# Kernel tuning notes

Measured on AMD Instinct MI355X. Metric: run time of the kernel, lower is better.

## Reference

```python
import jax, jax.numpy as jnp
import numpy as np

B, N = 256, 512          # trees, nodes per tree (topological order, root last)
IN, HID, OUT = 57, 512, 57  # len(ascii_letters + " .,;'") = 57


def setup_inputs() -> dict:
    rng = np.random.default_rng(0)
    # children indices strictly less than node index; -1 means absent child
    u = rng.random((B, N, 2))
    idx = np.arange(N)[None, :, None]
    ch = np.floor(u * (idx + 1)).astype(np.int32) - 1  # in [-1, i-1]
    left_idx = jnp.asarray(ch[..., 0])
    right_idx = jnp.asarray(ch[..., 1])
    values = jnp.asarray(rng.integers(0, IN, (B, N)), dtype=jnp.int32)
    key = jax.random.key(0)
    k1, k2, k3, k4 = jax.random.split(key, 4)
    s1 = 1.0 / np.sqrt(IN + HID)
    s2 = 1.0 / np.sqrt(HID)
    W_ih = jax.random.uniform(k1, (IN + HID, HID), minval=-s1, maxval=s1, dtype=jnp.float32)
    b_ih = jax.random.uniform(k2, (HID,), minval=-s1, maxval=s1, dtype=jnp.float32)
    W_o = jax.random.uniform(k3, (HID, OUT), minval=-s2, maxval=s2, dtype=jnp.float32)
    b_o = jax.random.uniform(k4, (OUT,), minval=-s2, maxval=s2, dtype=jnp.float32)
    return dict(left_idx=left_idx, right_idx=right_idx, values=values,
                W_ih=W_ih, b_ih=b_ih, W_o=W_o, b_o=b_o)


def _encode(left_idx, right_idx, values, W_ih, b_ih):
    # one-hot chars, precompute the input half of the concat+linear for all nodes
    X = jax.nn.one_hot(values, IN, dtype=W_ih.dtype)        # [B,N,IN]
    Wx, Wh = W_ih[:IN], W_ih[IN:]                            # split concat linear
    Xp = jnp.einsum('bni,ih->bnh', X, Wx) + b_ih             # [B,N,HID]
    SENT = N  # sentinel row holding zeros (hidden for None child)
    li = jnp.where(left_idx < 0, SENT, left_idx)             # [B,N]
    ri = jnp.where(right_idx < 0, SENT, right_idx)
    H0 = jnp.zeros((B, N + 1, HID), Xp.dtype)
    brange = jnp.arange(B)

    def step(H, inp):
        i, xp, l, r = inp                                    # xp:[B,HID], l/r:[B]
        hl = H[brange, l]                                    # gather child hiddens
        hr = H[brange, r]
        h = jnp.tanh(xp + (hl + hr) @ Wh)                    # recurrence
        H = H.at[:, i].set(h)
        return H, None

    xs = (jnp.arange(N), jnp.swapaxes(Xp, 0, 1), li.T, ri.T)
    H, _ = jax.lax.scan(step, H0, xs)
    return H[:, N - 1]                                       # root hidden [B,HID]


def reference(left_idx, right_idx, values, W_ih, b_ih, W_o, b_o):
    h_root = _encode(left_idx, right_idx, values, W_ih, b_ih)
    logits = h_root @ W_o + b_o                              # i2o
    return jax.nn.log_softmax(logits, axis=1)                # [B,OUT]
```

## Files before the change

### kernel.cpp

```cpp
#include <hip/hip_runtime.h>
#include <stdint.h>
#include <math.h>

#define BATCH 256
#define NNODE 512
#define INP   57
#define HIDD  512
#define OUTD  57
#define SENTOFF (NNODE * HIDD)

typedef int i32x4 __attribute__((ext_vector_type(4)));

__global__ void pack_wq(const float* __restrict__ W_ih, const float* __restrict__ b_ih,
                        signed char* __restrict__ Wq){
  int idx = blockIdx.x * 256 + threadIdx.x;
  int j    =  idx        & 15;
  int lane = (idx >> 4)  & 63;
  int nt   = (idx >> 10) & 31;
  int kt   =  idx >> 15;
  int n    = nt * 16 + (lane & 15);
  int ksub = (lane >> 4) * 16 + j;
  const float scale = 127.0f * sqrtf((float)(INP + HIDD));
  float wv; float sc = scale;
  if (kt < 8) {
    const int ktrue = kt * 64 + 16 * (ksub & 3) + (ksub >> 2);
    wv = W_ih[(size_t)(INP + ktrue) * HIDD + n];
  } else {
    sc = scale * 0.5f;
    if (ksub < INP)       wv = W_ih[(size_t)ksub * HIDD + n];
    else if (ksub == INP) wv = b_ih[n];
    else                  wv = 0.0f;
  }
  float q = rintf(wv * sc);
  q = fminf(127.0f, fmaxf(-127.0f, q));
  Wq[idx] = (signed char)q;
}

__device__ __forceinline__ unsigned int avg_s8x4(unsigned int a, unsigned int b){
  unsigned int au = a ^ 0x80808080u, bu = b ^ 0x80808080u;
  unsigned int o = au | bu, x = au ^ bu;
  return ((o - ((x >> 1) & 0x7F7F7F7Fu)) ^ 0x80808080u);
}

struct Pref { uint4 l[2]; uint4 r[2]; };

__device__ __forceinline__ void load_pref_safe(
    Pref& p, int m0, int Mcur, int w, int m16, int quad,
    const int* ord_s, const int* li_s, const int* ri_s, const int* hot_s,
    const signed char* Hb)
{
  const int koff = w * 64 + quad * 16;
  #pragma unroll
  for (int mt = 0; mt < 2; ++mt) {
    const int row  = mt * 16 + m16;
    const bool live = row < Mcur;
    const int pos  = m0 + row;
    const int node = live ? ord_s[pos] : -1;
    const int hb   = live ? hot_s[pos] : 0;
    const int loff = (node >= 0) ? li_s[node] : SENTOFF;
    const int roff = (node >= 0) ? ri_s[node] : SENTOFF;
    if (!(hb & 1)) p.l[mt] = *(const uint4*)(Hb + (size_t)(loff + koff));
    if (!(hb & 2)) p.r[mt] = *(const uint4*)(Hb + (size_t)(roff + koff));
  }
}

__device__ __forceinline__ void write_pref(
    const Pref& p, int m0, int Mcur, int w, int lane, int m16, int quad,
    signed char* __restrict__ Ab, const int* ord_s, const int* val_s)
{
  #pragma unroll
  for (int mt = 0; mt < 2; ++mt) {
    uint4 o;
    o.x = avg_s8x4(p.l[mt].x, p.r[mt].x);
    o.y = avg_s8x4(p.l[mt].y, p.r[mt].y);
    o.z = avg_s8x4(p.l[mt].z, p.r[mt].z);
    o.w = avg_s8x4(p.l[mt].w, p.r[mt].w);
    *(uint4*)(Ab + (w * 2 + mt) * 1024 + lane * 16) = o;
  }
  if (w < 2) {
    const int erow  = w * 16 + m16;
    const int enode = (erow < Mcur) ? ord_s[m0 + erow] : -1;
    const int v     = (enode >= 0) ? val_s[enode] : -1;
    signed char bytes[16];
    #pragma unroll
    for (int j = 0; j < 16; ++j) {
      const int ks = quad * 16 + j;
      bytes[j] = (enode >= 0 && (ks == v || ks == INP)) ? (signed char)127 : (signed char)0;
    }
    *(i32x4*)(Ab + (16 + w) * 1024 + lane * 16) = *(const i32x4*)bytes;
  }
}

__device__ __forceinline__ void patch_and_write(
    Pref& p, int m0, int Mcur, int w, int lane, int m16, int quad,
    signed char* __restrict__ Ab,
    const int* ord_s, const int* li_s, const int* ri_s, const int* val_s,
    const int* hot_s, const signed char* Hb)
{
  const int koff = w * 64 + quad * 16;
  #pragma unroll
  for (int mt = 0; mt < 2; ++mt) {
    const int row  = mt * 16 + m16;
    const bool live = row < Mcur;
    const int pos  = m0 + row;
    const int hb   = live ? hot_s[pos] : 0;
    if (hb) {
      const int node = ord_s[pos];
      if (hb & 1) p.l[mt] = *(const uint4*)(Hb + (size_t)(li_s[node] + koff));
      if (hb & 2) p.r[mt] = *(const uint4*)(Hb + (size_t)(ri_s[node] + koff));
    }
  }
  write_pref(p, m0, Mcur, w, lane, m16, quad, Ab, ord_s, val_s);
}

#define VSCALE_VAL (2.0f / (16129.0f * 23.853720883753127f))

__device__ __forceinline__ int tanh_q_lut(int accv, const signed char* lut){
  int idx = (accv + 655872) >> 10;
  idx = min(max(idx, 0), 1279);
  return lut[idx];
}

template<int NMT>
__device__ __forceinline__ void compute_chunk(
    int m0, int Mcur, int w, int lane, int m16, int quad,
    const signed char* __restrict__ Ab,
    const int* ordoff_s, const i32x4 (&Bv)[9][4], signed char* Hb,
    const signed char* __restrict__ lut)
{
  i32x4 acc[NMT][4];
  #pragma unroll
  for (int mt = 0; mt < NMT; ++mt)
    #pragma unroll
    for (int nt = 0; nt < 4; ++nt)
      acc[mt][nt] = (i32x4){0, 0, 0, 0};

  #pragma unroll
  for (int kt = 0; kt < 8; ++kt) {
    #pragma unroll
    for (int mt = 0; mt < NMT; ++mt) {
      i32x4 a = *(const i32x4*)(Ab + (kt * 2 + mt) * 1024 + lane * 16);
      #pragma unroll
      for (int nt = 0; nt < 4; ++nt)
        acc[mt][nt] = __builtin_amdgcn_mfma_i32_16x16x64_i8(a, Bv[kt][nt], acc[mt][nt], 0, 0, 0);
    }
  }
  #pragma unroll
  for (int mt = 0; mt < NMT; ++mt) {
    i32x4 ax = *(const i32x4*)(Ab + (16 + mt) * 1024 + lane * 16);
    #pragma unroll
    for (int nt = 0; nt < 4; ++nt)
      acc[mt][nt] = __builtin_amdgcn_mfma_i32_16x16x64_i8(ax, Bv[8][nt], acc[mt][nt], 0, 0, 0);
  }

  #pragma unroll
  for (int mt = 0; mt < NMT; ++mt) {
    #pragma unroll
    for (int rg = 0; rg < 4; ++rg) {
      const int rowc = mt * 16 + quad * 4 + rg;
      if (rowc < Mcur) {
        const int q0 = tanh_q_lut(acc[mt][0][rg], lut) & 255;
        const int q1 = tanh_q_lut(acc[mt][1][rg], lut) & 255;
        const int q2 = tanh_q_lut(acc[mt][2][rg], lut) & 255;
        const int q3 = tanh_q_lut(acc[mt][3][rg], lut);
        const int packed = q0 | (q1 << 8) | (q2 << 16) | (q3 << 24);
        *(int*)(Hb + (size_t)ordoff_s[m0 + rowc] + (w * 64 + m16 * 4)) = packed;
      }
    }
  }
}

__global__ __launch_bounds__(512, 2) void tree_rnn(
    const int* __restrict__ left, const int* __restrict__ right,
    const int* __restrict__ values,
    const float* __restrict__ W_ih, const float* __restrict__ b_ih,
    const float* __restrict__ W_o,  const float* __restrict__ b_o,
    const signed char* __restrict__ Wq,
    signed char* __restrict__ Hbuf, float* __restrict__ out)
{
  __shared__ __align__(16) signed char Abuf[2][18 * 1024];
  __shared__ signed char tanhlut_s[1280];
  __shared__ int li_s[NNODE], ri_s[NNODE], val_s[NNODE];
  __shared__ int lvl_s[NNODE], ord_s[NNODE], ordoff_s[NNODE], hot_s[NNODE];
  __shared__ int cnt_s[NNODE], cnt2_s[NNODE];
  __shared__ int offs_s[NNODE + 1];
  __shared__ int cdesc_s[NNODE];
  __shared__ int chg_s, lmax_s, nc_s;
  __shared__ float hroot_s[HIDD];
  __shared__ float red_s[OUTD][8];
  __shared__ float logit_s[64];

  const int b    = blockIdx.x;
  const int tid  = threadIdx.x;
  const int lane = tid & 63;
  const int w    = tid >> 6;
  signed char* Hb = Hbuf + (size_t)b * (NNODE + 1) * HIDD;

  li_s[tid]  = left  [b * NNODE + tid];
  ri_s[tid]  = right [b * NNODE + tid];
  val_s[tid] = values[b * NNODE + tid];
  lvl_s[tid] = 0; cnt_s[tid] = 0; cnt2_s[tid] = 0;
  if (tid < 128) ((unsigned int*)(Hb + (size_t)NNODE * HIDD))[tid] = 0;
  if (tid == 0) lmax_s = 0;
  for (int i = tid; i < 1280; i += 512) {
    const float xc = (float)((i << 10) - 655360) * VSCALE_VAL;
    tanhlut_s[i] = (signed char)__float2int_rn(127.0f * tanhf(xc));
  }
  __syncthreads();

  for (;;) {
    if (tid == 0) chg_s = 0;
    __syncthreads();
    {
      int l = li_s[tid], r = ri_s[tid];
      int dl = (l >= 0) ? lvl_s[l] : -1;
      int dr = (r >= 0) ? lvl_s[r] : -1;
      int nl = 1 + (dl > dr ? dl : dr);
      if (nl > lvl_s[tid]) { lvl_s[tid] = nl; chg_s = 1; }
    }
    __syncthreads();
    if (!chg_s) break;
  }

  const int myl = lvl_s[tid];
  {
    int ml = myl;
    #pragma unroll
    for (int m = 1; m < 64; m <<= 1) ml = max(ml, __shfl_xor(ml, m, 64));
    if (lane == 0) atomicMax(&lmax_s, ml);
    atomicAdd(&cnt_s[myl], 1);
  }
  __syncthreads();
  const int Lmax = lmax_s;
  if (tid == 0) {
    int acc = 0;
    for (int L = 0; L <= Lmax; ++L) { offs_s[L] = acc; acc += cnt_s[L]; }
    offs_s[Lmax + 1] = acc;
    int nc = 0;
    for (int L = 0; L <= Lmax; ++L)
      for (int m0 = offs_s[L]; m0 < offs_s[L + 1]; m0 += 32) {
        int sz = min(32, offs_s[L + 1] - m0);
        cdesc_s[nc++] = m0 | (sz << 16) | ((m0 == offs_s[L]) ? (1 << 30) : 0);
      }
    nc_s = nc;
  }
  __syncthreads();
  {
    int pos = offs_s[myl] + atomicAdd(&cnt2_s[myl], 1);
    ord_s[pos] = tid;
    ordoff_s[pos] = tid * HIDD;
  }
  __syncthreads();
  {
    const int node = ord_s[tid];
    const int L = lvl_s[node];
    const int l = li_s[node], r = ri_s[node];
    const bool first = (tid - offs_s[L]) < 32;
    int h = 0;
    if (first && l >= 0 && lvl_s[l] == L - 1) h |= 1;
    if (first && r >= 0 && lvl_s[r] == L - 1) h |= 2;
    hot_s[tid] = h;
  }
  __syncthreads();
  {
    int l = li_s[tid], r = ri_s[tid];
    li_s[tid] = (l < 0 ? NNODE : l) * HIDD;
    ri_s[tid] = (r < 0 ? NNODE : r) * HIDD;
  }
  __syncthreads();

  const int m16  = lane & 15;
  const int quad = lane >> 4;

  i32x4 Bv[9][4];
  #pragma unroll
  for (int kt = 0; kt < 9; ++kt)
    #pragma unroll
    for (int nt = 0; nt < 4; ++nt)
      Bv[kt][nt] = *(const i32x4*)(Wq + ((size_t)(kt * 32 + 4 * w + nt) * 64 + lane) * 16);

  const int NC = nc_s;
  Pref p;
  {
    const int d = cdesc_s[0];
    load_pref_safe(p, d & 0xFFFF, (d >> 16) & 0x3FFF, w, m16, quad,
                   ord_s, li_s, ri_s, hot_s, Hb);
  }
  for (int gc = 0; gc < NC; ++gc) {
    const int d  = cdesc_s[gc];
    const int m0 = d & 0xFFFF, Mc = (d >> 16) & 0x3FFF;
    const bool first = (d >> 30) & 1;
    __syncthreads();
    if (first) {
      patch_and_write(p, m0, Mc, w, lane, m16, quad, Abuf[gc & 1],
                      ord_s, li_s, ri_s, val_s, hot_s, Hb);
      __syncthreads();
    }
    const bool more = gc + 1 < NC;
    Pref pn; int m01 = 0, Mc1 = 0; bool f1 = false;
    if (more) {
      const int d1 = cdesc_s[gc + 1];
      m01 = d1 & 0xFFFF; Mc1 = (d1 >> 16) & 0x3FFF; f1 = (d1 >> 30) & 1;
      load_pref_safe(pn, m01, Mc1, w, m16, quad, ord_s, li_s, ri_s, hot_s, Hb);
    }
    const signed char* Ab = Abuf[gc & 1];
    if (Mc > 16)
      compute_chunk<2>(m0, Mc, w, lane, m16, quad, Ab, ordoff_s, Bv, Hb, tanhlut_s);
    else
      compute_chunk<1>(m0, Mc, w, lane, m16, quad, Ab, ordoff_s, Bv, Hb, tanhlut_s);
    if (more && !f1)
      write_pref(pn, m01, Mc1, w, lane, m16, quad, Abuf[(gc + 1) & 1], ord_s, val_s);
    p = pn;
  }
  __syncthreads();

  {
    const int t6 = tid & 63;
    const int tt = (tid & ~63) | (((t6 & 3) << 4) | (t6 >> 2));
    hroot_s[tt] = (float)Hb[(size_t)(NNODE - 1) * HIDD + tid] * (1.0f / 127.0f);
  }
  __syncthreads();
  {
    const int j = tid >> 3, part = tid & 7;
    if (j < OUTD) {
      float p2 = 0.f;
      const int k0 = part * 64;
      for (int k = k0; k < k0 + 64; ++k)
        p2 += hroot_s[k] * W_o[(size_t)k * OUTD + j];
      red_s[j][part] = p2;
    }
  }
  __syncthreads();
  if (tid < OUTD) {
    float s = b_o[tid];
    #pragma unroll
    for (int pp = 0; pp < 8; ++pp) s += red_s[tid][pp];
    logit_s[tid] = s;
  }
  __syncthreads();
  if (w == 0) {
    float x = (lane < OUTD) ? logit_s[lane] : -1e30f;
    float mx = x;
    #pragma unroll
    for (int m = 1; m < 64; m <<= 1) mx = fmaxf(mx, __shfl_xor(mx, m, 64));
    float ex = (lane < OUTD) ? __expf(x - mx) : 0.f;
    float sm = ex;
    #pragma unroll
    for (int m = 1; m < 64; m <<= 1) sm += __shfl_xor(sm, m, 64);
    float ls = logf(sm);
    if (lane < OUTD) out[b * OUTD + lane] = x - mx - ls;
  }
}

extern "C" void kernel_launch(void* const* d_in, const int* in_sizes, int n_in,
                              void* d_out, int out_size, void* d_ws, size_t ws_size,
                              hipStream_t stream) {
  const int*   left   = (const int*)  d_in[0];
  const int*   right  = (const int*)  d_in[1];
  const int*   values = (const int*)  d_in[2];
  const float* W_ih   = (const float*)d_in[3];
  const float* b_ih   = (const float*)d_in[4];
  const float* W_o    = (const float*)d_in[5];
  const float* b_o    = (const float*)d_in[6];
  float* out = (float*)d_out;

  signed char* Wq   = (signed char*)d_ws;
  signed char* Hbuf = (signed char*)((char*)d_ws + 512 * 1024);

  pack_wq<<<1152, 256, 0, stream>>>(W_ih, b_ih, Wq);
  tree_rnn<<<BATCH, 512, 0, stream>>>(left, right, values, W_ih, b_ih, W_o, b_o,
                                      Wq, Hbuf, out);
}
```

Baseline: 199.0 us.

## Process two trees per workgroup and interleave their level chunks

Each workgroup now handles two trees, loading the quantized weight fragments into registers once and interleaving the chunk computations of both trees inside one loop with shared barriers. The intent is to amortize the per-block weight register load and the barrier latency across two independent recurrences, so the memory and sync stalls of one tree can be hidden by work on the other. The cost is half as many blocks (128 on a GPU with many more CUs), doubled LDS use, and serialized work per block, which may leave much of the device idle.

```diff
diff --git a/kernel.cpp b/kernel.cpp
--- a/kernel.cpp
+++ b/kernel.cpp
@@ -178,14 +178,14 @@
     const signed char* __restrict__ Wq,
     signed char* __restrict__ Hbuf, float* __restrict__ out)
 {
-  __shared__ __align__(16) signed char Abuf[2][18 * 1024];
+  __shared__ __align__(16) signed char Abuf[2][2][18 * 1024];
   __shared__ signed char tanhlut_s[1280];
-  __shared__ int li_s[NNODE], ri_s[NNODE], val_s[NNODE];
-  __shared__ int lvl_s[NNODE], ord_s[NNODE], ordoff_s[NNODE], hot_s[NNODE];
-  __shared__ int cnt_s[NNODE], cnt2_s[NNODE];
-  __shared__ int offs_s[NNODE + 1];
-  __shared__ int cdesc_s[NNODE];
-  __shared__ int chg_s, lmax_s, nc_s;
+  __shared__ int li_s[2][NNODE], ri_s[2][NNODE], val_s[2][NNODE];
+  __shared__ int lvl_s[2][NNODE], ord_s[2][NNODE], ordoff_s[2][NNODE], hot_s[2][NNODE];
+  __shared__ int cnt_s[2][NNODE], cnt2_s[2][NNODE];
+  __shared__ int offs_s[2][NNODE + 1];
+  __shared__ int cdesc_s[2][NNODE];
+  __shared__ int chg_s, lmax_s[2], nc_s[2];
   __shared__ float hroot_s[HIDD];
   __shared__ float red_s[OUTD][8];
   __shared__ float logit_s[64];
@@ -194,14 +194,20 @@
   const int tid  = threadIdx.x;
   const int lane = tid & 63;
   const int w    = tid >> 6;
-  signed char* Hb = Hbuf + (size_t)b * (NNODE + 1) * HIDD;
-
-  li_s[tid]  = left  [b * NNODE + tid];
-  ri_s[tid]  = right [b * NNODE + tid];
-  val_s[tid] = values[b * NNODE + tid];
-  lvl_s[tid] = 0; cnt_s[tid] = 0; cnt2_s[tid] = 0;
-  if (tid < 128) ((unsigned int*)(Hb + (size_t)NNODE * HIDD))[tid] = 0;
-  if (tid == 0) lmax_s = 0;
+  signed char* HbT[2] = {
+    Hbuf + (size_t)(2 * b)     * (NNODE + 1) * HIDD,
+    Hbuf + (size_t)(2 * b + 1) * (NNODE + 1) * HIDD };
+
+  #pragma unroll
+  for (int t = 0; t < 2; ++t) {
+    const int r = (2 * b + t) * NNODE + tid;
+    li_s[t][tid]  = left[r];
+    ri_s[t][tid]  = right[r];
+    val_s[t][tid] = values[r];
+    lvl_s[t][tid] = 0; cnt_s[t][tid] = 0; cnt2_s[t][tid] = 0;
+    if (tid < 128) ((unsigned int*)(HbT[t] + (size_t)NNODE * HIDD))[tid] = 0;
+  }
+  if (tid < 2) lmax_s[tid] = 0;
   for (int i = tid; i < 1280; i += 512) {
     const float xc = (float)((i << 10) - 655360) * VSCALE_VAL;
     tanhlut_s[i] = (signed char)__float2int_rn(127.0f * tanhf(xc));
@@ -211,61 +217,69 @@
   for (;;) {
     if (tid == 0) chg_s = 0;
     __syncthreads();
-    {
-      int l = li_s[tid], r = ri_s[tid];
-      int dl = (l >= 0) ? lvl_s[l] : -1;
-      int dr = (r >= 0) ? lvl_s[r] : -1;
+    int any = 0;
+    #pragma unroll
+    for (int t = 0; t < 2; ++t) {
+      int l = li_s[t][tid], r = ri_s[t][tid];
+      int dl = (l >= 0) ? lvl_s[t][l] : -1;
+      int dr = (r >= 0) ? lvl_s[t][r] : -1;
       int nl = 1 + (dl > dr ? dl : dr);
-      if (nl > lvl_s[tid]) { lvl_s[tid] = nl; chg_s = 1; }
-    }
+      if (nl > lvl_s[t][tid]) { lvl_s[t][tid] = nl; any = 1; }
+    }
+    if (any) chg_s = 1;
     __syncthreads();
     if (!chg_s) break;
   }
 
-  const int myl = lvl_s[tid];
-  {
-    int ml = myl;
+  #pragma unroll
+  for (int t = 0; t < 2; ++t) {
+    int ml = lvl_s[t][tid];
     #pragma unroll
     for (int m = 1; m < 64; m <<= 1) ml = max(ml, __shfl_xor(ml, m, 64));
-    if (lane == 0) atomicMax(&lmax_s, ml);
-    atomicAdd(&cnt_s[myl], 1);
-  }
-  __syncthreads();
-  const int Lmax = lmax_s;
-  if (tid == 0) {
+    if (lane == 0) atomicMax(&lmax_s[t], ml);
+    atomicAdd(&cnt_s[t][lvl_s[t][tid]], 1);
+  }
+  __syncthreads();
+  if (tid < 2) {
+    const int t = tid;
     int acc = 0;
-    for (int L = 0; L <= Lmax; ++L) { offs_s[L] = acc; acc += cnt_s[L]; }
-    offs_s[Lmax + 1] = acc;
+    const int Lm = lmax_s[t];
+    for (int L = 0; L <= Lm; ++L) { offs_s[t][L] = acc; acc += cnt_s[t][L]; }
+    offs_s[t][Lm + 1] = acc;
     int nc = 0;
-    for (int L = 0; L <= Lmax; ++L)
-      for (int m0 = offs_s[L]; m0 < offs_s[L + 1]; m0 += 32) {
-        int sz = min(32, offs_s[L + 1] - m0);
-        cdesc_s[nc++] = m0 | (sz << 16) | ((m0 == offs_s[L]) ? (1 << 30) : 0);
+    for (int L = 0; L <= Lm; ++L)
+      for (int m0 = offs_s[t][L]; m0 < offs_s[t][L + 1]; m0 += 32) {
+        int sz = min(32, offs_s[t][L + 1] - m0);
+        cdesc_s[t][nc++] = m0 | (sz << 16) | ((m0 == offs_s[t][L]) ? (1 << 30) : 0);
       }
-    nc_s = nc;
-  }
-  __syncthreads();
-  {
-    int pos = offs_s[myl] + atomicAdd(&cnt2_s[myl], 1);
-    ord_s[pos] = tid;
-    ordoff_s[pos] = tid * HIDD;
-  }
-  __syncthreads();
-  {
-    const int node = ord_s[tid];
-    const int L = lvl_s[node];
-    const int l = li_s[node], r = ri_s[node];
-    const bool first = (tid - offs_s[L]) < 32;
+    nc_s[t] = nc;
+  }
+  __syncthreads();
+  #pragma unroll
+  for (int t = 0; t < 2; ++t) {
+    const int myl = lvl_s[t][tid];
+    int pos = offs_s[t][myl] + atomicAdd(&cnt2_s[t][myl], 1);
+    ord_s[t][pos] = tid;
+    ordoff_s[t][pos] = tid * HIDD;
+  }
+  __syncthreads();
+  #pragma unroll
+  for (int t = 0; t < 2; ++t) {
+    const int node = ord_s[t][tid];
+    const int L = lvl_s[t][node];
+    const int l = li_s[t][node], r = ri_s[t][node];
+    const bool first = (tid - offs_s[t][L]) < 32;
     int h = 0;
-    if (first && l >= 0 && lvl_s[l] == L - 1) h |= 1;
-    if (first && r >= 0 && lvl_s[r] == L - 1) h |= 2;
-    hot_s[tid] = h;
-  }
-  __syncthreads();
-  {
-    int l = li_s[tid], r = ri_s[tid];
-    li_s[tid] = (l < 0 ? NNODE : l) * HIDD;
-    ri_s[tid] = (r < 0 ? NNODE : r) * HIDD;
+    if (first && l >= 0 && lvl_s[t][l] == L - 1) h |= 1;
+    if (first && r >= 0 && lvl_s[t][r] == L - 1) h |= 2;
+    hot_s[t][tid] = h;
+  }
+  __syncthreads();
+  #pragma unroll
+  for (int t = 0; t < 2; ++t) {
+    int l = li_s[t][tid], r = ri_s[t][tid];
+    li_s[t][tid] = (l < 0 ? NNODE : l) * HIDD;
+    ri_s[t][tid] = (r < 0 ? NNODE : r) * HIDD;
   }
   __syncthreads();
 
@@ -279,76 +293,110 @@
     for (int nt = 0; nt < 4; ++nt)
       Bv[kt][nt] = *(const i32x4*)(Wq + ((size_t)(kt * 32 + 4 * w + nt) * 64 + lane) * 16);
 
-  const int NC = nc_s;
-  Pref p;
+  const int NCa = nc_s[0], NCb = nc_s[1];
+  const int NC = max(NCa, NCb);
+  Pref pA, pB;
   {
-    const int d = cdesc_s[0];
-    load_pref_safe(p, d & 0xFFFF, (d >> 16) & 0x3FFF, w, m16, quad,
-                   ord_s, li_s, ri_s, hot_s, Hb);
+    const int d = cdesc_s[0][0];
+    load_pref_safe(pA, d & 0xFFFF, (d >> 16) & 0x3FFF, w, m16, quad,
+                   ord_s[0], li_s[0], ri_s[0], hot_s[0], HbT[0]);
+    const int e = cdesc_s[1][0];
+    load_pref_safe(pB, e & 0xFFFF, (e >> 16) & 0x3FFF, w, m16, quad,
+                   ord_s[1], li_s[1], ri_s[1], hot_s[1], HbT[1]);
   }
   for (int gc = 0; gc < NC; ++gc) {
-    const int d  = cdesc_s[gc];
-    const int m0 = d & 0xFFFF, Mc = (d >> 16) & 0x3FFF;
-    const bool first = (d >> 30) & 1;
-    __syncthreads();
-    if (first) {
-      patch_and_write(p, m0, Mc, w, lane, m16, quad, Abuf[gc & 1],
-                      ord_s, li_s, ri_s, val_s, hot_s, Hb);
-      __syncthreads();
-    }
-    const bool more = gc + 1 < NC;
-    Pref pn; int m01 = 0, Mc1 = 0; bool f1 = false;
-    if (more) {
-      const int d1 = cdesc_s[gc + 1];
-      m01 = d1 & 0xFFFF; Mc1 = (d1 >> 16) & 0x3FFF; f1 = (d1 >> 30) & 1;
-      load_pref_safe(pn, m01, Mc1, w, m16, quad, ord_s, li_s, ri_s, hot_s, Hb);
-    }
-    const signed char* Ab = Abuf[gc & 1];
-    if (Mc > 16)
-      compute_chunk<2>(m0, Mc, w, lane, m16, quad, Ab, ordoff_s, Bv, Hb, tanhlut_s);
-    else
-      compute_chunk<1>(m0, Mc, w, lane, m16, quad, Ab, ordoff_s, Bv, Hb, tanhlut_s);
-    if (more && !f1)
-      write_pref(pn, m01, Mc1, w, lane, m16, quad, Abuf[(gc + 1) & 1], ord_s, val_s);
-    p = pn;
-  }
-  __syncthreads();
-
-  {
-    const int t6 = tid & 63;
-    const int tt = (tid & ~63) | (((t6 & 3) << 4) | (t6 >> 2));
-    hroot_s[tt] = (float)Hb[(size_t)(NNODE - 1) * HIDD + tid] * (1.0f / 127.0f);
-  }
-  __syncthreads();
-  {
-    const int j = tid >> 3, part = tid & 7;
-    if (j < OUTD) {
-      float p2 = 0.f;
-      const int k0 = part * 64;
-      for (int k = k0; k < k0 + 64; ++k)
-        p2 += hroot_s[k] * W_o[(size_t)k * OUTD + j];
-      red_s[j][part] = p2;
-    }
-  }
-  __syncthreads();
-  if (tid < OUTD) {
-    float s = b_o[tid];
-    #pragma unroll
-    for (int pp = 0; pp < 8; ++pp) s += red_s[tid][pp];
-    logit_s[tid] = s;
-  }
-  __syncthreads();
-  if (w == 0) {
-    float x = (lane < OUTD) ? logit_s[lane] : -1e30f;
-    float mx = x;
-    #pragma unroll
-    for (int m = 1; m < 64; m <<= 1) mx = fmaxf(mx, __shfl_xor(mx, m, 64));
-    float ex = (lane < OUTD) ? __expf(x - mx) : 0.f;
-    float sm = ex;
-    #pragma unroll
-    for (int m = 1; m < 64; m <<= 1) sm += __shfl_xor(sm, m, 64);
-    float ls = logf(sm);
-    if (lane < OUTD) out[b * OUTD + lane] = x - mx - ls;
+    const int dA = (gc < NCa) ? cdesc_s[0][gc] : 0;
+    const int dB = (gc < NCb) ? cdesc_s[1][gc] : 0;
+    const bool fA = (gc < NCa) && ((dA >> 30) & 1);
+    const bool fB = (gc < NCb) && ((dB >> 30) & 1);
+    __syncthreads();
+    if (fA) patch_and_write(pA, dA & 0xFFFF, (dA >> 16) & 0x3FFF, w, lane, m16, quad,
+                            &Abuf[0][gc & 1][0], ord_s[0], li_s[0], ri_s[0],
+                            val_s[0], hot_s[0], HbT[0]);
+    if (fB) patch_and_write(pB, dB & 0xFFFF, (dB >> 16) & 0x3FFF, w, lane, m16, quad,
+                            &Abuf[1][gc & 1][0], ord_s[1], li_s[1], ri_s[1],
+                            val_s[1], hot_s[1], HbT[1]);
+    if (fA | fB) __syncthreads();
+
+    if (gc < NCa) {
+      const int m0 = dA & 0xFFFF, Mc = (dA >> 16) & 0x3FFF;
+      const bool more = gc + 1 < NCa;
+      int m01 = 0, Mc1 = 0; bool f1 = false;
+      if (more) {
+        const int d1 = cdesc_s[0][gc + 1];
+        m01 = d1 & 0xFFFF; Mc1 = (d1 >> 16) & 0x3FFF; f1 = (d1 >> 30) & 1;
+        load_pref_safe(pA, m01, Mc1, w, m16, quad,
+                       ord_s[0], li_s[0], ri_s[0], hot_s[0], HbT[0]);
+      }
+      const signed char* Ab = &Abuf[0][gc & 1][0];
+      if (Mc > 16)
+        compute_chunk<2>(m0, Mc, w, lane, m16, quad, Ab, ordoff_s[0], Bv, HbT[0], tanhlut_s);
+      else
+        compute_chunk<1>(m0, Mc, w, lane, m16, quad, Ab, ordoff_s[0], Bv, HbT[0], tanhlut_s);
+      if (more && !f1)
+        write_pref(pA, m01, Mc1, w, lane, m16, quad,
+                   &Abuf[0][(gc + 1) & 1][0], ord_s[0], val_s[0]);
+    }
+    if (gc < NCb) {
+      const int m0 = dB & 0xFFFF, Mc = (dB >> 16) & 0x3FFF;
+      const bool more = gc + 1 < NCb;
+      int m01 = 0, Mc1 = 0; bool f1 = false;
+      if (more) {
+        const int d1 = cdesc_s[1][gc + 1];
+        m01 = d1 & 0xFFFF; Mc1 = (d1 >> 16) & 0x3FFF; f1 = (d1 >> 30) & 1;
+        load_pref_safe(pB, m01, Mc1, w, m16, quad,
+                       ord_s[1], li_s[1], ri_s[1], hot_s[1], HbT[1]);
+      }
+      const signed char* Ab = &Abuf[1][gc & 1][0];
+      if (Mc > 16)
+        compute_chunk<2>(m0, Mc, w, lane, m16, quad, Ab, ordoff_s[1], Bv, HbT[1], tanhlut_s);
+      else
+        compute_chunk<1>(m0, Mc, w, lane, m16, quad, Ab, ordoff_s[1], Bv, HbT[1], tanhlut_s);
+      if (more && !f1)
+        write_pref(pB, m01, Mc1, w, lane, m16, quad,
+                   &Abuf[1][(gc + 1) & 1][0], ord_s[1], val_s[1]);
+    }
+  }
+  __syncthreads();
+
+  for (int t = 0; t < 2; ++t) {
+    {
+      const int t6 = tid & 63;
+      const int tt = (tid & ~63) | (((t6 & 3) << 4) | (t6 >> 2));
+      hroot_s[tt] = (float)HbT[t][(size_t)(NNODE - 1) * HIDD + tid] * (1.0f / 127.0f);
+    }
+    __syncthreads();
+    {
+      const int j = tid >> 3, part = tid & 7;
+      if (j < OUTD) {
+        float p2 = 0.f;
+        const int k0 = part * 64;
+        for (int k = k0; k < k0 + 64; ++k)
+          p2 += hroot_s[k] * W_o[(size_t)k * OUTD + j];
+        red_s[j][part] = p2;
+      }
+    }
+    __syncthreads();
+    if (tid < OUTD) {
+      float s = b_o[tid];
+      #pragma unroll
+      for (int pp = 0; pp < 8; ++pp) s += red_s[tid][pp];
+      logit_s[tid] = s;
+    }
+    __syncthreads();
+    if (w == 0) {
+      float x = (lane < OUTD) ? logit_s[lane] : -1e30f;
+      float mx = x;
+      #pragma unroll
+      for (int m = 1; m < 64; m <<= 1) mx = fmaxf(mx, __shfl_xor(mx, m, 64));
+      float ex = (lane < OUTD) ? __expf(x - mx) : 0.f;
+      float sm = ex;
+      #pragma unroll
+      for (int m = 1; m < 64; m <<= 1) sm += __shfl_xor(sm, m, 64);
+      float ls = logf(sm);
+      if (lane < OUTD) out[(2 * b + t) * OUTD + lane] = x - mx - ls;
+    }
+    __syncthreads();
   }
 }
 
@@ -368,6 +416,6 @@
   signed char* Hbuf = (signed char*)((char*)d_ws + 512 * 1024);
 
   pack_wq<<<1152, 256, 0, stream>>>(W_ih, b_ih, Wq);
-  tree_rnn<<<BATCH, 512, 0, stream>>>(left, right, values, W_ih, b_ih, W_o, b_o,
-                                      Wq, Hbuf, out);
-}
+  tree_rnn<<<BATCH / 2, 512, 0, stream>>>(left, right, values, W_ih, b_ih, W_o, b_o,
+                                          Wq, Hbuf, out);
+}
```

Measured after the change: 329.3 us. 1.65x slower.
